# Performance work log

Hardware: AMD Instinct MI355X
Metric: run time of the kernel (lower is better)

Reference implementation:

```python
import jax, jax.numpy as jnp
import numpy as np
from jax import lax

STRIDES = [8, 16, 32, 64, 128]
NUM_CLASSES = 80
PRE_NMS_THRESH = 0.05
PRE_NMS_TOP_N = 1000
NMS_THRESH = 0.6
MAX_DET = 100
IMG_SIZE = 800.0
BBOX_W = (10.0, 10.0, 5.0, 5.0)
SCALE_CLAMP = float(np.log(1000.0 / 16.0))  # Box2BoxTransform clamp


def conv3x3(x, w, b):
    y = lax.conv_general_dilated(x, w, (1, 1), 'SAME',
                                 dimension_numbers=('NCHW', 'OIHW', 'NCHW'))
    return y + b[None, :, None, None]


def conv1x1(x, w, b):
    return jnp.einsum('nchw,kc->nkhw', x, w) + b[None, :, None, None]


def make_anchors(H, W, stride):
    # one square anchor per location, size = 8 * stride (ATSS), offset 0.5
    size = 8.0 * stride
    xs = (jnp.arange(W, dtype=jnp.float32) + 0.5) * stride
    ys = (jnp.arange(H, dtype=jnp.float32) + 0.5) * stride
    cy, cx = jnp.meshgrid(ys, xs, indexing='ij')
    half = size / 2.0
    return jnp.stack([cx - half, cy - half, cx + half, cy + half], -1).reshape(-1, 4)


def decode(deltas, anchors):
    # Box2BoxTransform.apply_deltas with weights (10,10,5,5)
    wx, wy, ww, wh = BBOX_W
    aw = anchors[..., 2] - anchors[..., 0]
    ah = anchors[..., 3] - anchors[..., 1]
    acx = anchors[..., 0] + 0.5 * aw
    acy = anchors[..., 1] + 0.5 * ah
    dx = deltas[..., 0] / wx
    dy = deltas[..., 1] / wy
    dw = jnp.minimum(deltas[..., 2] / ww, SCALE_CLAMP)
    dh = jnp.minimum(deltas[..., 3] / wh, SCALE_CLAMP)
    pcx = dx * aw + acx
    pcy = dy * ah + acy
    pw = jnp.exp(dw) * aw
    ph = jnp.exp(dh) * ah
    boxes = jnp.stack([pcx - 0.5 * pw, pcy - 0.5 * ph,
                       pcx + 0.5 * pw, pcy + 0.5 * ph], -1)
    return jnp.clip(boxes, 0.0, IMG_SIZE)


def iou_one_vs_all(box, boxes):
    x1 = jnp.maximum(box[0], boxes[:, 0])
    y1 = jnp.maximum(box[1], boxes[:, 1])
    x2 = jnp.minimum(box[2], boxes[:, 2])
    y2 = jnp.minimum(box[3], boxes[:, 3])
    inter = jnp.clip(x2 - x1, 0.0) * jnp.clip(y2 - y1, 0.0)
    a1 = (box[2] - box[0]) * (box[3] - box[1])
    a2 = (boxes[:, 2] - boxes[:, 0]) * (boxes[:, 3] - boxes[:, 1])
    return inter / (a1 + a2 - inter + 1e-9)


def nms_single(boxes, scores, classes):
    # class-aware greedy NMS via per-class coordinate offset (ml_nms trick)
    off = classes.astype(boxes.dtype)[:, None] * (2.0 * IMG_SIZE)
    ob = boxes + off

    def step(s, _):
        i = jnp.argmax(s)
        best = s[i]
        iou = iou_one_vs_all(ob[i], ob)
        s = jnp.where(iou > NMS_THRESH, -1.0, s)
        s = s.at[i].set(-1.0)
        return s, (i, best)

    _, (idx, kept) = lax.scan(step, scores, None, length=MAX_DET)
    valid = kept > 0
    out_boxes = jnp.where(valid[:, None], boxes[idx], 0.0)
    out_scores = jnp.where(valid, kept, 0.0)
    out_classes = jnp.where(valid, classes[idx], -1)
    return out_boxes, out_scores, out_classes


def atss_forward(feats, cls_tw, cls_tb, bbox_tw, bbox_tb,
                 wcls, bcls, wbox, bbox_b, wctr, bctr, scales):
    all_boxes, all_scores, all_classes = [], [], []
    for l, x in enumerate(feats):
        c = x
        b = x
        for i in range(cls_tw.shape[0]):  # 4 tower convs
            c = jax.nn.relu(conv3x3(c, cls_tw[i], cls_tb[i]))
            b = jax.nn.relu(conv3x3(b, bbox_tw[i], bbox_tb[i]))
        logits = conv1x1(c, wcls, bcls)               # [N,C,H,W]
        deltas = scales[l] * conv1x1(b, wbox, bbox_b)  # [N,4,H,W]
        ctr = conv1x1(b, wctr, bctr)                   # [N,1,H,W]
        N, C, H, W = logits.shape
        logits = logits.transpose(0, 2, 3, 1).reshape(N, H * W, C)
        deltas = deltas.transpose(0, 2, 3, 1).reshape(N, H * W, 4)
        ctr = ctr.transpose(0, 2, 3, 1).reshape(N, H * W)
        anchors = make_anchors(H, W, STRIDES[l])       # [HW,4]
        # ATSS inference scoring: sigmoid(cls) * sigmoid(centerness)
        s = jax.nn.sigmoid(logits) * jax.nn.sigmoid(ctr)[..., None]
        s = jnp.where(s > PRE_NMS_THRESH, s, 0.0)
        flat = s.reshape(N, -1)                        # [N, HW*C]
        k = min(PRE_NMS_TOP_N, flat.shape[1])
        vals, idx = lax.top_k(flat, k)
        aidx = idx // C
        cidx = idx % C
        d = jnp.take_along_axis(deltas, aidx[:, :, None], axis=1)  # [N,k,4]
        boxes = decode(d, anchors[aidx])
        # final score = sqrt(cls*ctr); safe sqrt to avoid inf grad at 0
        sc = jnp.sqrt(jnp.where(vals > 0, vals, 1.0)) * (vals > 0)
        all_boxes.append(boxes)
        all_scores.append(sc)
        all_classes.append(cidx)
    boxes = jnp.concatenate(all_boxes, 1)
    scores = jnp.concatenate(all_scores, 1)
    classes = jnp.concatenate(all_classes, 1)
    return jax.vmap(nms_single)(boxes, scores, classes)


def setup_inputs() -> dict:
    key = jax.random.key(0)
    ks = jax.random.split(key, 12)
    feats_hw = [(100, 100), (50, 50), (25, 25), (13, 13), (7, 7)]
    N, CIN, CH = 4, 256, 256
    inp = {}
    for i, (h, w) in enumerate(feats_hw):
        inp['p%d' % (i + 3)] = jax.random.normal(ks[i], (N, CIN, h, w), jnp.float32)
    inp['cls_tw'] = jax.random.normal(ks[5], (4, CH, CIN, 3, 3), jnp.float32) * 0.02
    inp['cls_tb'] = jnp.zeros((4, CH), jnp.float32)
    inp['bbox_tw'] = jax.random.normal(ks[6], (4, CH, CIN, 3, 3), jnp.float32) * 0.02
    inp['bbox_tb'] = jnp.zeros((4, CH), jnp.float32)
    inp['wcls'] = jax.random.normal(ks[7], (NUM_CLASSES, CH), jnp.float32) * 0.05
    inp['bcls'] = jnp.zeros((NUM_CLASSES,), jnp.float32)
    inp['wbox'] = jax.random.normal(ks[8], (4, CH), jnp.float32) * 0.05
    inp['bbox_b'] = jnp.zeros((4,), jnp.float32)
    inp['wctr'] = jax.random.normal(ks[9], (1, CH), jnp.float32) * 0.05
    inp['bctr'] = jnp.zeros((1,), jnp.float32)
    inp['scales'] = jnp.ones((5,), jnp.float32)
    return inp


def reference(p3, p4, p5, p6, p7, cls_tw, cls_tb, bbox_tw, bbox_tb,
              wcls, bcls, wbox, bbox_b, wctr, bctr, scales):
    feats = [p3, p4, p5, p6, p7]
    boxes, scores, classes = atss_forward(feats, cls_tw, cls_tb, bbox_tw, bbox_tb,
                                          wcls, bcls, wbox, bbox_b, wctr, bctr, scales)
    return boxes, scores, classes
```

## Files before the change

kernel.cpp:

```cpp
#include <hip/hip_runtime.h>
#include <math.h>

typedef short s8v __attribute__((ext_vector_type(8)));
typedef short s4v __attribute__((ext_vector_type(4)));
typedef float f4v __attribute__((ext_vector_type(4)));
typedef _Float16 h8v __attribute__((ext_vector_type(8)));

__device__ __forceinline__ float sigf(float x) { return 1.f / (1.f + expf(-x)); }
__device__ __forceinline__ float f16f(short v) {
  return (float)__builtin_bit_cast(_Float16, v);
}

#define SCALE_CLAMP 4.135166556742356f
#define IMG_SIZE 800.f
#define PLANE 14482432ull
#define W_SCALE 1024.f
#define A_SCALE 64.f
#define ACC_RESCALE 1.52587890625e-5f

__device__ __forceinline__ void split2(float x, short& h, short& l) {
  _Float16 hf = (_Float16)x;
  _Float16 lf = (_Float16)(x - (float)hf);
  h = __builtin_bit_cast(short, hf);
  l = __builtin_bit_cast(short, lf);
}

struct Geo {
  int tp[6];
  int TXa[5];
  int Ha[5], Wa[5], PWa[5], PHWa[5];
  int phwOff[5];
  int hwOff[5];
  int pb[6];
  int bb[6];
};

__global__ __launch_bounds__(256) void wtrans_k(const float* __restrict__ cls_tw,
                                                const float* __restrict__ bbox_tw,
                                                short* __restrict__ wt)
{
  const int total = 589824;
  for (int u = blockIdx.x * 256 + threadIdx.x; u < total; u += gridDim.x * 256) {
    int layer = u / 73728;
    int r = u - layer * 73728;
    int tap = r / 8192;  r -= tap * 8192;
    int cc  = r / 1024;  r -= cc * 1024;
    int qq  = r / 256;   int ko = r - qq * 256;
    int cibase = cc * 32 + qq * 8;
    const float* src = (layer < 4) ? (cls_tw + (size_t)layer * 589824)
                                   : (bbox_tw + (size_t)(layer - 4) * 589824);
    s8v hv, lv;
#pragma unroll
    for (int e = 0; e < 8; ++e) {
      float x = src[(size_t)ko * 2304 + (size_t)(cibase + e) * 9 + tap] * W_SCALE;
      short h, l; split2(x, h, l);
      hv[e] = h; lv[e] = l;
    }
    size_t dbase = (size_t)layer * 1179648 + (((size_t)tap * 8 + cc) * 4 + qq) * 2048 + (size_t)ko * 8;
    *(s8v*)(wt + dbase) = hv;
    *(s8v*)(wt + dbase + 589824) = lv;
  }
}

__global__ __launch_bounds__(256) void prep_all_k(const float* __restrict__ p3, const float* __restrict__ p4,
                                                  const float* __restrict__ p5, const float* __restrict__ p6,
                                                  const float* __restrict__ p7,
                                                  short* __restrict__ out, Geo g)
{
  __shared__ float tl[64][260];
  int bx = blockIdx.x, t = threadIdx.x, n = blockIdx.y;
  int l = 0; while (l < 4 && bx >= g.pb[l + 1]) ++l;
  const float* in = (l == 0) ? p3 : (l == 1) ? p4 : (l == 2) ? p5 : (l == 3) ? p6 : p7;
  int H = g.Ha[l], W = g.Wa[l], PW = g.PWa[l], PHW = g.PHWa[l], HW = H * W;
  int P0 = (bx - g.pb[l]) * 64;
  const float* inN = in + (size_t)n * HW * 256;
  int sub = t >> 6, pl = t & 63;
  int pos = P0 + pl;
  for (int i = 0; i < 64; ++i) {
    int ci = i * 4 + sub;
    tl[pl][ci] = (pos < HW) ? inN[(size_t)ci * HW + pos] : 0.f;
  }
  __syncthreads();
  int pl2 = t >> 2, cq = (t & 3) * 64;
  int pos2 = P0 + pl2;
  if (pos2 < HW) {
    int y = pos2 / W, x = pos2 - y * W;
    size_t oo = ((size_t)g.phwOff[l] * 4 + (size_t)n * PHW + (size_t)(y + 1) * PW + (x + 1)) * 256 + cq;
#pragma unroll
    for (int grp = 0; grp < 8; ++grp) {
      s8v hv, lv;
#pragma unroll
      for (int e = 0; e < 8; ++e) {
        short h, lo; split2(tl[pl2][cq + grp * 8 + e] * A_SCALE, h, lo);
        hv[e] = h; lv[e] = lo;
      }
      *(s8v*)(out + oo + grp * 8) = hv;
      *(s8v*)(out + PLANE + oo + grp * 8) = lv;
    }
  }
}

#define QS    128
#define PSTR  4096
#define BSTR  8192
__global__ __launch_bounds__(256, 4) void conv_all_k(const short* __restrict__ in0,
                                                     const short* __restrict__ wtL,
                                                     const float* __restrict__ bias,
                                                     short* __restrict__ out0, Geo g)
{
  __shared__ short act_s[2 * BSTR];

  const int t = threadIdx.x;
  const int lane = t & 63, wave = t >> 6;
  const int wcol = wave & 1, wko = wave >> 1;
  const int nT = g.tp[5];
  int bid = blockIdx.x;
  int wgid = (bid & 7) * nT + (bid >> 3);
  const int n = wgid / (2 * nT);
  int r2 = wgid - n * 2 * nT;
  int bx = r2 >> 1;
  const int ko0 = (r2 & 1) * 128;
  int l = 0; while (l < 4 && bx >= g.tp[l + 1]) ++l;
  const int H = g.Ha[l], W = g.Wa[l], PW = g.PWa[l], PHW = g.PHWa[l];
  const int lt = bx - g.tp[l];
  const int TX = g.TXa[l];
  const int ty = lt / TX, tx = lt - ty * TX;
  const int R0 = ty * 4, C0 = tx * 16;
  const size_t bi = ((size_t)g.phwOff[l] * 4 + (size_t)n * PHW) * 256;
  const short* inN = in0 + bi;
  short* outN = out0 + bi;

  const int r = lane & 15, q = lane >> 4;
  const int cb = wcol * 8;
  const short* wlane = wtL + (size_t)q * 2048 + (size_t)(ko0 + wko * 64 + r) * 8;
  const int abase = q * QS + 2 * q + (r >> 3) * 18 + cb + (r & 7);

  int soff[2];
#pragma unroll
  for (int k = 0; k < 2; ++k) {
    int j = t + k * 256;
    int qq = j >> 7, ppos = j & 127;
    int lpos = ppos - 2 * qq;
    if (lpos < 0) lpos = 0;
    if (lpos > 107) lpos = 107;
    int row = lpos / 18, col = lpos - row * 18;
    int prow = R0 + row; if (prow > H + 1) prow = H + 1;
    int pcol = C0 + col; if (pcol > W + 1) pcol = W + 1;
    soff[k] = (prow * PW + pcol) * 256 + qq * 8;
  }

  f4v acc[2][4];
#pragma unroll
  for (int mi = 0; mi < 2; ++mi)
#pragma unroll
    for (int ni = 0; ni < 4; ++ni) { f4v z = {0.f, 0.f, 0.f, 0.f}; acc[mi][ni] = z; }

  auto stage = [&](int cc, int buf) {
#pragma unroll
    for (int k = 0; k < 2; ++k)
#pragma unroll
      for (int p = 0; p < 2; ++p) {
        const short* src = inN + (size_t)p * PLANE + (size_t)(soff[k] + cc * 32);
        short* dst = &act_s[(size_t)buf * BSTR + (size_t)p * PSTR + (size_t)(t + k * 256) * 8];
#if __has_builtin(__builtin_amdgcn_global_load_lds)
        __builtin_amdgcn_global_load_lds((const __attribute__((address_space(1))) void*)src,
                                         (__attribute__((address_space(3))) void*)dst, 16, 0, 0);
#else
        *(s8v*)dst = *(const s8v*)src;
#endif
      }
  };

  auto loadW = [&](s8v (&w)[2][2], int cc2, int tap2, int half) {
    const short* base = wlane + (size_t)(tap2 * 8 + cc2) * 8192 + half * 256;
#pragma unroll
    for (int p = 0; p < 2; ++p)
#pragma unroll
      for (int k = 0; k < 2; ++k)
        w[p][k] = *(const s8v*)(base + (size_t)p * 589824 + k * 128);
  };

  auto loadA = [&](s8v (&af)[2][2], int dy, int dx, int buf) {
    const int b0 = buf * BSTR + abase * 8;
    const int d = (dy * 18 + dx) * 8;
#pragma unroll
    for (int mi = 0; mi < 2; ++mi) {
      af[0][mi] = *(const s8v*)&act_s[b0 + mi * 288 + d];
      af[1][mi] = *(const s8v*)&act_s[b0 + PSTR + mi * 288 + d];
    }
  };

  auto runHalf = [&](const s8v (&w)[2][2], const s8v (&af)[2][2], int half) {
    const int PA[3] = {0, 0, 1};
    const int PB[3] = {0, 1, 0};
    __builtin_amdgcn_s_setprio(1);
#pragma unroll
    for (int pp = 0; pp < 3; ++pp)
#pragma unroll
      for (int mi = 0; mi < 2; ++mi)
#pragma unroll
        for (int k = 0; k < 2; ++k)
          acc[mi][half * 2 + k] = __builtin_amdgcn_mfma_f32_16x16x32_f16(
              __builtin_bit_cast(h8v, af[PA[pp]][mi]),
              __builtin_bit_cast(h8v, w[PB[pp]][k]),
              acc[mi][half * 2 + k], 0, 0, 0);
    __builtin_amdgcn_s_setprio(0);
  };

  s8v wH0[2][2], wH1[2][2], afr[2][2];
  stage(0, 0);
  loadW(wH0, 0, 0, 0);
  __syncthreads();

  int cur = 0;
  for (int cc = 0; cc < 8; ++cc) {
    if (cc < 7) stage(cc + 1, cur ^ 1);
#pragma unroll
    for (int tap = 0; tap < 9; ++tap) {
      const int dy = tap / 3, dx = tap - dy * 3;
      loadW(wH1, cc, tap, 1);
      loadA(afr, dy, dx, cur);
      runHalf(wH0, afr, 0);
      int ntap = tap + 1, ncc = cc;
      if (ntap == 9) { ntap = 0; ++ncc; }
      if (ncc < 8) loadW(wH0, ncc, ntap, 0);
      runHalf(wH1, afr, 1);
    }
    __syncthreads();
    cur ^= 1;
  }

#pragma unroll
  for (int mi = 0; mi < 2; ++mi) {
#pragma unroll
    for (int ni = 0; ni < 4; ++ni) {
      int ko = ko0 + wko * 64 + ni * 16 + r;
      float bv = bias[ko];
#pragma unroll
      for (int reg = 0; reg < 4; ++reg) {
        int rm = q * 4 + reg;
        int orow = R0 + 2 * mi + (rm >> 3);
        int ocol = C0 + cb + (rm & 7);
        if (orow < H && ocol < W) {
          float real = acc[mi][ni][reg] * ACC_RESCALE + bv;
          float vv = fmaxf(real, 0.f) * A_SCALE;
          short h, lo; split2(vv, h, lo);
          size_t oo = ((size_t)(orow + 1) * PW + (ocol + 1)) * 256 + ko;
          outN[oo] = h; outN[PLANE + oo] = lo;
        }
      }
    }
  }
}

__global__ __launch_bounds__(256) void cls_head_k(const short* __restrict__ act,
                                                  const float* __restrict__ wcls,
                                                  const float* __restrict__ bcls,
                                                  float* __restrict__ score, Geo g)
{
  __shared__ int   p2s[64];
  __shared__ float as_[64][69];
  __shared__ float ws_[64][84];
  const int t = threadIdx.x;
  const int n = blockIdx.y;
  int bx = blockIdx.x;
  int l = 0; while (l < 4 && bx >= g.pb[l + 1]) ++l;
  const int H = g.Ha[l], W = g.Wa[l], PW = g.PWa[l], PHW = g.PHWa[l], HW = H * W;
  const int P0 = (bx - g.pb[l]) * 64;
  if (t < 64) {
    int p = P0 + t; if (p >= HW) p = HW - 1;
    int y = p / W, x = p - y * W;
    p2s[t] = (y + 1) * PW + x + 1;
  }
  __syncthreads();
  float accv[4][5];
#pragma unroll
  for (int i = 0; i < 4; ++i)
#pragma unroll
    for (int j = 0; j < 5; ++j) accv[i][j] = 0.f;

  const short* actN = act + ((size_t)g.phwOff[l] * 4 + (size_t)n * PHW) * 256;
  const int pg = t >> 4, cg = t & 15;
  const float inv = 1.f / A_SCALE;

  for (int c0 = 0; c0 < 256; c0 += 64) {
    for (int i = t; i < 1024; i += 256) {
      int pos = i >> 4, c4 = i & 15;
      size_t o = (size_t)p2s[pos] * 256 + c0 + c4 * 4;
      s4v hv = *(const s4v*)(actN + o);
      s4v lv = *(const s4v*)(actN + PLANE + o);
      float* dst = &as_[pos][c4 * 4];
#pragma unroll
      for (int e = 0; e < 4; ++e) dst[e] = (f16f(hv[e]) + f16f(lv[e])) * inv;
    }
    for (int i = t; i < 1280; i += 256) {
      int c = i >> 4, c4 = i & 15;
      float4 v = *(const float4*)(wcls + (size_t)c * 256 + c0 + c4 * 4);
      ws_[c4 * 4 + 0][c] = v.x; ws_[c4 * 4 + 1][c] = v.y;
      ws_[c4 * 4 + 2][c] = v.z; ws_[c4 * 4 + 3][c] = v.w;
    }
    __syncthreads();
#pragma unroll 8
    for (int ci = 0; ci < 64; ++ci) {
#pragma unroll
      for (int i = 0; i < 4; ++i) {
        float a = as_[pg * 4 + i][ci];
#pragma unroll
        for (int j = 0; j < 5; ++j)
          accv[i][j] = fmaf(a, ws_[ci][cg * 5 + j], accv[i][j]);
      }
    }
    __syncthreads();
  }
  float* sB = score + ((size_t)g.hwOff[l] * 4 + (size_t)n * HW) * 80;
#pragma unroll
  for (int i = 0; i < 4; ++i) {
    int p = P0 + pg * 4 + i;
    if (p >= HW) continue;
#pragma unroll
    for (int j = 0; j < 5; ++j) {
      int c = cg * 5 + j;
      sB[(size_t)p * 80 + c] = sigf(accv[i][j] + bcls[c]);
    }
  }
}

__global__ __launch_bounds__(256) void box_head_k(const short* __restrict__ act,
                                                  const float* __restrict__ wbox,
                                                  const float* __restrict__ bb,
                                                  const float* __restrict__ wctr,
                                                  const float* __restrict__ bc,
                                                  const float* __restrict__ scales,
                                                  float* __restrict__ score,
                                                  float* __restrict__ deltas, Geo g)
{
  int n = blockIdx.y;
  int bx = blockIdx.x;
  int l = 0; while (l < 4 && bx >= g.bb[l + 1]) ++l;
  const int H = g.Ha[l], W = g.Wa[l], PW = g.PWa[l], PHW = g.PHWa[l], HW = H * W;
  int p = (bx - g.bb[l]) * 256 + threadIdx.x;
  if (p >= HW) return;
  int y = p / W, x = p - y * W;
  const short* a = act + ((size_t)g.phwOff[l] * 4 + (size_t)n * PHW + (size_t)(y + 1) * PW + x + 1) * 256;
  const float inv = 1.f / A_SCALE;
  float d0 = 0, d1 = 0, d2 = 0, d3 = 0, ct = 0;
  for (int gI = 0; gI < 32; ++gI) {
    s8v hv = *(const s8v*)(a + gI * 8);
    s8v lv = *(const s8v*)(a + PLANE + gI * 8);
#pragma unroll
    for (int e = 0; e < 8; ++e) {
      float av = (f16f(hv[e]) + f16f(lv[e])) * inv;
      int c = gI * 8 + e;
      d0 = fmaf(av, wbox[c], d0);
      d1 = fmaf(av, wbox[256 + c], d1);
      d2 = fmaf(av, wbox[512 + c], d2);
      d3 = fmaf(av, wbox[768 + c], d3);
      ct = fmaf(av, wctr[c], ct);
    }
  }
  float sl = scales[l];
  float* dd = deltas + ((size_t)g.hwOff[l] * 4 + (size_t)n * HW + p) * 4;
  dd[0] = sl * (d0 + bb[0]); dd[1] = sl * (d1 + bb[1]);
  dd[2] = sl * (d2 + bb[2]); dd[3] = sl * (d3 + bb[3]);
  float sct = sigf(ct + bc[0]);
  float* sp = score + ((size_t)g.hwOff[l] * 4 + (size_t)n * HW + p) * 80;
#pragma unroll
  for (int i = 0; i < 20; ++i) {
    float4 v = ((float4*)sp)[i];
    v.x *= sct; v.y *= sct; v.z *= sct; v.w *= sct;
    v.x = (v.x > 0.05f) ? v.x : 0.f;
    v.y = (v.y > 0.05f) ? v.y : 0.f;
    v.z = (v.z > 0.05f) ? v.z : 0.f;
    v.w = (v.w > 0.05f) ? v.w : 0.f;
    ((float4*)sp)[i] = v;
  }
}

__global__ __launch_bounds__(256) void hist_k(const float* __restrict__ score,
                                              const unsigned* __restrict__ thr,
                                              unsigned* __restrict__ hist, int phase, Geo g)
{
  const int grp = blockIdx.y;
  const int l = grp >> 2, n = grp & 3;
  const int HW = g.Ha[l] * g.Wa[l];
  const int M = HW * 80;
  const float* s = score + ((size_t)g.hwOff[l] * 4 + (size_t)n * HW) * 80;
  unsigned* h = hist + grp * 2048;
  const unsigned* tr = thr + grp * 8;
  __shared__ unsigned lh[2048];
  for (int i = threadIdx.x; i < 2048; i += 256) lh[i] = 0u;
  __syncthreads();
  unsigned B1 = 0, pref = 0;
  if (phase == 1) B1 = tr[0];
  if (phase == 2) pref = (tr[0] << 11) | tr[1];
  for (int idx = blockIdx.x * 256 + threadIdx.x; idx < M; idx += gridDim.x * 256) {
    float v = s[idx];
    if (v > 0.f) {
      unsigned b = __float_as_uint(v);
      if (phase == 0) atomicAdd(&lh[b >> 20], 1u);
      else if (phase == 1) { if ((b >> 20) == B1) atomicAdd(&lh[(b >> 9) & 0x7FFu], 1u); }
      else { if ((b >> 9) == pref) atomicAdd(&lh[b & 0x1FFu], 1u); }
    }
  }
  __syncthreads();
  for (int i = threadIdx.x; i < 2048; i += 256) { unsigned v = lh[i]; if (v) atomicAdd(&h[i], v); }
}

__global__ __launch_bounds__(256) void scan_k(unsigned* __restrict__ hist,
                                              unsigned* __restrict__ thr, int phase)
{
  const int grp = blockIdx.x, t = threadIdx.x;
  unsigned* h  = hist + grp * 2048;
  unsigned* tr = thr + grp * 8;
  const int nb = (phase == 2) ? 512 : 2048;
  const int PB = nb / 256;
  unsigned target = 1000u;
  bool dead = false;
  if (phase >= 1) {
    target = 1000u - tr[2];
    if (tr[0] == 0xFFFFFFFFu) dead = true;
    if (phase == 2 && tr[1] == 0xFFFFFFFFu) dead = true;
  }
  __shared__ unsigned ps[256];
  __shared__ unsigned s_tot;
  const int hi = nb - t * PB;
  unsigned lsum = 0;
  for (int k = 0; k < PB; ++k) lsum += h[hi - 1 - k];
  ps[t] = lsum;
  __syncthreads();
  if (t == 0) {
    unsigned cum = 0;
    for (int i = 0; i < 256; ++i) { unsigned tmp = ps[i]; ps[i] = cum; cum += tmp; }
    s_tot = cum;
  }
  __syncthreads();
  unsigned exc = ps[t], tot = s_tot;
  if (!dead && tot >= target) {
    if (exc < target && exc + lsum >= target) {
      unsigned cum = exc; int bf = 0; unsigned above = 0;
      for (int k = 0; k < PB; ++k) {
        int bidx = hi - 1 - k;
        unsigned c = h[bidx];
        if (cum < target && cum + c >= target) { bf = bidx; above = cum; }
        cum += c;
      }
      if (phase == 0)      { tr[0] = (unsigned)bf; tr[2] = above; }
      else if (phase == 1) { tr[1] = (unsigned)bf; tr[2] = tr[2] + above; }
      else {
        unsigned T = (tr[0] << 20) | (tr[1] << 9) | (unsigned)bf;
        tr[3] = T; tr[4] = target - above;
      }
    }
  } else if (t == 0) {
    if (phase == 0)      { tr[0] = 0xFFFFFFFFu; tr[2] = 0u; }
    else if (phase == 1) { tr[1] = 0xFFFFFFFFu; }
    else                 { tr[3] = 0u; tr[4] = 0u; }
  }
  if (phase == 2 && t == 0) { tr[5] = 0u; tr[6] = 0u; }
}

__global__ __launch_bounds__(256) void select_k(const float* __restrict__ score,
                                                const float* __restrict__ deltas,
                                                unsigned* __restrict__ thr,
                                                float* __restrict__ cbox, float* __restrict__ csc,
                                                float* __restrict__ ccls, float* __restrict__ cgid,
                                                Geo g)
{
  const int grp = blockIdx.y;
  const int l = grp >> 2, n = grp & 3;
  const int W = g.Wa[l];
  const int HW = g.Ha[l] * W;
  const int M = HW * 80;
  const float stride_ = (float)(8 << l);
  const float* s = score + ((size_t)g.hwOff[l] * 4 + (size_t)n * HW) * 80;
  const float* dBase = deltas + ((size_t)g.hwOff[l] * 4 + (size_t)n * HW) * 4;
  unsigned* tr = thr + grp * 8;
  const unsigned T = tr[3], need = tr[4];
  for (int idx = blockIdx.x * 256 + threadIdx.x; idx < M; idx += gridDim.x * 256) {
    float v = s[idx];
    if (!(v > 0.f)) continue;
    unsigned b = __float_as_uint(v);
    int slot = -1;
    if (b > T) slot = (int)atomicAdd(&tr[5], 1u);
    else if (b == T) {
      unsigned e = atomicAdd(&tr[6], 1u);
      if (e < need) slot = (int)(1000u - need + e);
    }
    if (slot < 0) continue;
    int p = idx / 80, c = idx - p * 80;
    int y = p / W, x = p - y * W;
    const float* d = dBase + (size_t)p * 4;
    float sz  = 8.f * stride_;
    float acx = ((float)x + 0.5f) * stride_;
    float acy = ((float)y + 0.5f) * stride_;
    float dx = d[0] / 10.f, dy = d[1] / 10.f;
    float dw = fminf(d[2] / 5.f, SCALE_CLAMP);
    float dh = fminf(d[3] / 5.f, SCALE_CLAMP);
    float pcx = dx * sz + acx;
    float pcy = dy * sz + acy;
    float pw = expf(dw) * sz;
    float ph = expf(dh) * sz;
    float x1 = pcx - 0.5f * pw, y1_ = pcy - 0.5f * ph;
    float x2 = pcx + 0.5f * pw, y2_ = pcy + 0.5f * ph;
    x1  = fminf(fmaxf(x1, 0.f),  IMG_SIZE);
    y1_ = fminf(fmaxf(y1_, 0.f), IMG_SIZE);
    x2  = fminf(fmaxf(x2, 0.f),  IMG_SIZE);
    y2_ = fminf(fmaxf(y2_, 0.f), IMG_SIZE);
    int cslot = n * 5000 + l * 1000 + slot;
    ((float4*)cbox)[cslot] = make_float4(x1, y1_, x2, y2_);
    csc[cslot]  = sqrtf(v);
    ccls[cslot] = (float)c;
    cgid[cslot] = (float)(((unsigned)l << 20) | (unsigned)idx);
  }
}

__global__ __launch_bounds__(256) void nms_bucket_k(const float* __restrict__ cbox,
                                                    const float* __restrict__ csc,
                                                    const float* __restrict__ ccls,
                                                    const float* __restrict__ cgid,
                                                    float4* __restrict__ bbox2,
                                                    unsigned long long* __restrict__ bkey2,
                                                    int* __restrict__ coff)
{
  __shared__ unsigned cnt[80];
  __shared__ unsigned off_s[81];
  const int n = blockIdx.x, t = threadIdx.x;
  for (int i = t; i < 80; i += 256) cnt[i] = 0u;
  __syncthreads();
  for (int i = t; i < 5000; i += 256) {
    float s = csc[n * 5000 + i];
    if (s > 0.f) atomicAdd(&cnt[(int)ccls[n * 5000 + i]], 1u);
  }
  __syncthreads();
  if (t == 0) {
    unsigned c = 0;
    for (int k = 0; k < 80; ++k) { off_s[k] = c; c += cnt[k]; }
    off_s[80] = c;
  }
  __syncthreads();
  for (int i = t; i < 81; i += 256) coff[n * 81 + i] = (int)off_s[i];
  for (int i = t; i < 80; i += 256) cnt[i] = 0u;
  __syncthreads();
  for (int i = t; i < 5000; i += 256) {
    float s = csc[n * 5000 + i];
    if (s > 0.f) {
      int c = (int)ccls[n * 5000 + i];
      unsigned p = atomicAdd(&cnt[c], 1u);
      int dst = n * 5000 + (int)off_s[c] + (int)p;
      bbox2[dst] = ((const float4*)cbox)[n * 5000 + i];
      unsigned long long sb = (unsigned long long)__float_as_uint(s);
      unsigned gid = (unsigned)cgid[n * 5000 + i];
      bkey2[dst] = (sb << 24) | (unsigned long long)(0xFFFFFFu - gid);
    }
  }
}

#define NCAP 1536
__global__ __launch_bounds__(64) void nms_class_k(const float4* __restrict__ bbox2,
                                                  unsigned long long* __restrict__ bkey2,
                                                  const int* __restrict__ coff,
                                                  float4* __restrict__ kbox,
                                                  unsigned long long* __restrict__ kkey,
                                                  int* __restrict__ kcnt)
{
  __shared__ unsigned long long key_s[NCAP];
  __shared__ unsigned long long sk_s[NCAP];
  __shared__ float4 sb_s[NCAP];
  __shared__ unsigned char af_s[NCAP + 64];
  const int cls = blockIdx.x, n = blockIdx.y, t = threadIdx.x;
  const int lo = coff[n * 81 + cls], hi = coff[n * 81 + cls + 1];
  const int c = hi - lo;
  const int base = n * 5000 + lo;
  const int outB = (n * 80 + cls) * 100;
  int kept = 0;
  if (c > 0 && c <= NCAP) {
    const int nch = (c + 63) >> 6;
    for (int i = t; i < nch * 64; i += 64) af_s[i] = 0;
    for (int i = t; i < c; i += 64) key_s[i] = bkey2[base + i];
    __syncthreads();
    for (int i = t; i < c; i += 64) {
      unsigned long long ki = key_s[i];
      int rk = 0;
      for (int m = 0; m < c; ++m) rk += (key_s[m] > ki) ? 1 : 0;
      sk_s[rk] = ki;
      sb_s[rk] = bbox2[base + i];
      af_s[rk] = 1;
    }
    __syncthreads();
    int p = -1;
    while (kept < 100) {
      int np = -1;
      int j0 = (p + 1) >> 6;
      for (int j = j0; j < nch; ++j) {
        int pos = j * 64 + t;
        unsigned long long w = __ballot(af_s[pos] != 0);
        if (j == j0) { int sh = (p + 1) & 63; if (sh) w &= (~0ull) << sh; }
        if (w) { np = j * 64 + (int)__builtin_ctzll(w); break; }
      }
      if (np < 0) break;
      p = np;
      float4 wb = sb_s[p];
      if (t == 0) { kbox[outB + kept] = wb; kkey[outB + kept] = sk_s[p]; }
      ++kept;
      float a1 = (wb.z - wb.x) * (wb.w - wb.y);
      for (int i = p + t; i < c; i += 64) {
        if (!af_s[i]) continue;
        float4 b = sb_s[i];
        float xx1 = fmaxf(wb.x, b.x), yy1 = fmaxf(wb.y, b.y);
        float xx2 = fminf(wb.z, b.z), yy2 = fminf(wb.w, b.w);
        float inter = fmaxf(xx2 - xx1, 0.f) * fmaxf(yy2 - yy1, 0.f);
        float a2 = (b.z - b.x) * (b.w - b.y);
        if (inter / (a1 + a2 - inter + 1e-9f) > 0.6f) af_s[i] = 0;
      }
      __syncthreads();
    }
  } else if (c > NCAP) {
    while (kept < 100) {
      unsigned long long best = 0ull; int bi = 0;
      for (int i = t; i < c; i += 64) {
        unsigned long long k = bkey2[base + i];
        if (k > best) { best = k; bi = i; }
      }
#pragma unroll
      for (int o = 32; o; o >>= 1) {
        unsigned long long ok = __shfl_xor(best, o);
        int oi = __shfl_xor(bi, o);
        if (ok > best) { best = ok; bi = oi; }
      }
      if (best == 0ull) break;
      float4 wb = bbox2[base + bi];
      if (t == 0) { kbox[outB + kept] = wb; kkey[outB + kept] = best; }
      ++kept;
      float a1 = (wb.z - wb.x) * (wb.w - wb.y);
      for (int i = t; i < c; i += 64) {
        unsigned long long k = bkey2[base + i];
        if (!k) continue;
        float4 b = bbox2[base + i];
        float xx1 = fmaxf(wb.x, b.x), yy1 = fmaxf(wb.y, b.y);
        float xx2 = fminf(wb.z, b.z), yy2 = fminf(wb.w, b.w);
        float inter = fmaxf(xx2 - xx1, 0.f) * fmaxf(yy2 - yy1, 0.f);
        float a2 = (b.z - b.x) * (b.w - b.y);
        if (inter / (a1 + a2 - inter + 1e-9f) > 0.6f) bkey2[base + i] = 0ull;
      }
      __syncthreads();
    }
  }
  if (t == 0) kcnt[n * 80 + cls] = kept;
}

__global__ __launch_bounds__(64) void nms_merge_k(const float4* __restrict__ kbox,
                                                  const unsigned long long* __restrict__ kkey,
                                                  const int* __restrict__ kcnt,
                                                  float* __restrict__ outp)
{
  __shared__ unsigned long long lk[8000];
  __shared__ int head[80];
  __shared__ int cnts[80];
  const int n = blockIdx.x, t = threadIdx.x;
  for (int i = t; i < 80; i += 64) { head[i] = 0; cnts[i] = kcnt[n * 80 + i]; }
  for (int i = t; i < 8000; i += 64) lk[i] = kkey[n * 8000 + i];
  __syncthreads();
  for (int it = 0; it < 100; ++it) {
    unsigned long long best = 0ull; int bc = 0;
    for (int cls = t; cls < 80; cls += 64) {
      int h = head[cls];
      if (h < cnts[cls]) {
        unsigned long long k = lk[cls * 100 + h];
        if (k > best) { best = k; bc = cls; }
      }
    }
#pragma unroll
    for (int o = 32; o; o >>= 1) {
      unsigned long long ok = __shfl_xor(best, o);
      int oc = __shfl_xor(bc, o);
      if (ok > best) { best = ok; bc = oc; }
    }
    if (t == 0) {
      int basei = n * 100 + it;
      if (best != 0ull) {
        int idx = (n * 80 + bc) * 100 + head[bc];
        float4 b = kbox[idx];
        outp[basei * 4 + 0] = b.x; outp[basei * 4 + 1] = b.y;
        outp[basei * 4 + 2] = b.z; outp[basei * 4 + 3] = b.w;
        outp[1600 + basei] = __uint_as_float((unsigned)(best >> 24));
        outp[2000 + basei] = (float)bc;
        head[bc] = head[bc] + 1;
      } else {
        outp[basei * 4 + 0] = 0.f; outp[basei * 4 + 1] = 0.f;
        outp[basei * 4 + 2] = 0.f; outp[basei * 4 + 3] = 0.f;
        outp[1600 + basei] = 0.f;
        outp[2000 + basei] = -1.f;
      }
    }
    __syncthreads();
  }
}

extern "C" void kernel_launch(void* const* d_in, const int* in_sizes, int n_in,
                              void* d_out, int out_size, void* d_ws, size_t ws_size,
                              hipStream_t stream)
{
  (void)in_sizes; (void)n_in; (void)out_size; (void)ws_size;
  const float* p3 = (const float*)d_in[0];
  const float* p4 = (const float*)d_in[1];
  const float* p5 = (const float*)d_in[2];
  const float* p6 = (const float*)d_in[3];
  const float* p7 = (const float*)d_in[4];
  const float* cls_tw  = (const float*)d_in[5];
  const float* cls_tb  = (const float*)d_in[6];
  const float* bbox_tw = (const float*)d_in[7];
  const float* bbox_tb = (const float*)d_in[8];
  const float* wcls    = (const float*)d_in[9];
  const float* bcls    = (const float*)d_in[10];
  const float* wbox    = (const float*)d_in[11];
  const float* bbox_b  = (const float*)d_in[12];
  const float* wctr    = (const float*)d_in[13];
  const float* bctr    = (const float*)d_in[14];
  const float* scales  = (const float*)d_in[15];
  float* out = (float*)d_out;

  Geo G;
  const int Hs[5] = {100, 50, 25, 13, 7};
  {
    int tpre = 0, ppre = 0, bpre = 0, phw = 0, hw = 0;
    for (int l = 0; l < 5; ++l) {
      int H = Hs[l], W = Hs[l];
      G.Ha[l] = H; G.Wa[l] = W; G.PWa[l] = W + 2; G.PHWa[l] = (H + 2) * (W + 2);
      G.TXa[l] = (W + 15) / 16;
      int TY = (H + 3) / 4;
      G.tp[l] = tpre;  tpre += G.TXa[l] * TY;
      G.pb[l] = ppre;  ppre += (H * W + 63) / 64;
      G.bb[l] = bpre;  bpre += (H * W + 255) / 256;
      G.phwOff[l] = phw; phw += G.PHWa[l];
      G.hwOff[l]  = hw;  hw  += H * W;
    }
    G.tp[5] = tpre; G.pb[5] = ppre; G.bb[5] = bpre;
  }
  const int nTiles = G.tp[5];
  const int nPrep  = G.pb[5];
  const int nBoxB  = G.bb[5];
  const int sumHW = 13343;
  const size_t scoreBytes  = (size_t)sumHW * 4 * 80 * 4;
  const size_t deltasBytes = (size_t)sumHW * 4 * 4 * 4;

  char* ws = (char*)d_ws;
  size_t off = 0;
  auto alloc = [&](size_t bytes) -> void* {
    off = (off + 255) & ~(size_t)255;
    void* p = ws + off; off += bytes; return p;
  };
  const size_t bufBytes = 2ull * PLANE * 2;

  short* wt     = (short*)alloc((size_t)8 * 2 * 589824 * 2);
  float* cbox   = (float*)alloc(4ull * 5000 * 4 * 4);
  float* csc    = (float*)alloc(4ull * 5000 * 4);
  float* ccls   = (float*)alloc(4ull * 5000 * 4);
  float* cgid   = (float*)alloc(4ull * 5000 * 4);
  unsigned* hist = (unsigned*)alloc(20ull * 2048 * 4);
  unsigned* thr  = (unsigned*)alloc(20ull * 8 * 4);
  float4* bbox2 = (float4*)alloc(4ull * 5000 * 16);
  unsigned long long* bkey2 = (unsigned long long*)alloc(4ull * 5000 * 8);
  int* coff     = (int*)alloc(4ull * 81 * 4);
  float4* kbox  = (float4*)alloc(320ull * 100 * 16);
  unsigned long long* kkey = (unsigned long long*)alloc(320ull * 100 * 8);
  int* kcnt     = (int*)alloc(320ull * 4);
  short* C = (short*)alloc(bufBytes);
  short* A = (short*)alloc(bufBytes);
  short* B = (short*)alloc(bufBytes);
  float* score  = (float*)alloc(scoreBytes);
  float* deltas = (float*)alloc(deltasBytes);

  hipMemsetAsync(csc,  0, 4ull * 5000 * 4, stream);
  hipMemsetAsync(ccls, 0, 4ull * 5000 * 4, stream);
  hipMemsetAsync(cgid, 0, 4ull * 5000 * 4, stream);
  hipMemsetAsync(thr,  0, 20ull * 8 * 4, stream);
  hipMemsetAsync(C, 0, bufBytes, stream);
  hipMemsetAsync(A, 0, bufBytes, stream);
  hipMemsetAsync(B, 0, bufBytes, stream);

  wtrans_k<<<1024, 256, 0, stream>>>(cls_tw, bbox_tw, wt);

  const size_t LSTRIDE = 2ull * 589824;
  dim3 cg(8 * nTiles);

  prep_all_k<<<dim3(nPrep, 4), 256, 0, stream>>>(p3, p4, p5, p6, p7, C, G);
  conv_all_k<<<cg, 256, 0, stream>>>(C, wt + 0 * LSTRIDE, cls_tb + 0 * 256, A, G);
  conv_all_k<<<cg, 256, 0, stream>>>(A, wt + 1 * LSTRIDE, cls_tb + 1 * 256, B, G);
  conv_all_k<<<cg, 256, 0, stream>>>(B, wt + 2 * LSTRIDE, cls_tb + 2 * 256, A, G);
  conv_all_k<<<cg, 256, 0, stream>>>(A, wt + 3 * LSTRIDE, cls_tb + 3 * 256, B, G);
  cls_head_k<<<dim3(nPrep, 4), 256, 0, stream>>>(B, wcls, bcls, score, G);
  conv_all_k<<<cg, 256, 0, stream>>>(C, wt + 4 * LSTRIDE, bbox_tb + 0 * 256, A, G);
  conv_all_k<<<cg, 256, 0, stream>>>(A, wt + 5 * LSTRIDE, bbox_tb + 1 * 256, C, G);
  conv_all_k<<<cg, 256, 0, stream>>>(C, wt + 6 * LSTRIDE, bbox_tb + 2 * 256, A, G);
  conv_all_k<<<cg, 256, 0, stream>>>(A, wt + 7 * LSTRIDE, bbox_tb + 3 * 256, C, G);
  box_head_k<<<dim3(nBoxB, 4), 256, 0, stream>>>(C, wbox, bbox_b, wctr, bctr, scales,
                                                 score, deltas, G);

  const int hb = 196;
  for (int phase = 0; phase < 3; ++phase) {
    hipMemsetAsync(hist, 0, 20ull * 2048 * 4, stream);
    hist_k<<<dim3(hb, 20), 256, 0, stream>>>(score, thr, hist, phase, G);
    scan_k<<<20, 256, 0, stream>>>(hist, thr, phase);
  }
  select_k<<<dim3(hb, 20), 256, 0, stream>>>(score, deltas, thr, cbox, csc, ccls, cgid, G);

  nms_bucket_k<<<4, 256, 0, stream>>>(cbox, csc, ccls, cgid, bbox2, bkey2, coff);
  nms_class_k<<<dim3(80, 4), 64, 0, stream>>>(bbox2, bkey2, coff, kbox, kkey, kcnt);
  nms_merge_k<<<4, 64, 0, stream>>>(kbox, kkey, kcnt, out);
}
```

Measured before the change: 2.165 ms.

## Prefetch full next-tap weights into ping-pong registers in conv kernel

Restructures the conv main loop so each tap loads the full set of weight fragments for the next tap into an alternating register buffer, instead of splitting weights into two halves. Each tap now runs all of its MFMAs back to back, with a scheduling barrier keeping the prefetch loads ahead of the compute. The channel-chunk loop is unrolled in pairs so the buffer roles swap statically. This needs more registers, so the launch bound drops from 4 to 3 waves per SIMD, trading occupancy for deeper load latency hiding.

```diff
diff --git a/kernel.cpp b/kernel.cpp
--- a/kernel.cpp
+++ b/kernel.cpp
@@ -103,7 +103,7 @@
 #define QS    128
 #define PSTR  4096
 #define BSTR  8192
-__global__ __launch_bounds__(256, 4) void conv_all_k(const short* __restrict__ in0,
+__global__ __launch_bounds__(256, 3) void conv_all_k(const short* __restrict__ in0,
                                                      const short* __restrict__ wtL,
                                                      const float* __restrict__ bias,
                                                      short* __restrict__ out0, Geo g)
@@ -171,26 +171,24 @@
       }
   };
 
-  auto loadW = [&](s8v (&w)[2][2], int cc2, int tap2, int half) {
-    const short* base = wlane + (size_t)(tap2 * 8 + cc2) * 8192 + half * 256;
+  auto loadWT = [&](s8v (&w)[2][4], int cc2, int tap2) {
+    const short* base = wlane + (size_t)(tap2 * 8 + cc2) * 8192;
 #pragma unroll
     for (int p = 0; p < 2; ++p)
 #pragma unroll
-      for (int k = 0; k < 2; ++k)
+      for (int k = 0; k < 4; ++k)
         w[p][k] = *(const s8v*)(base + (size_t)p * 589824 + k * 128);
   };
 
-  auto loadA = [&](s8v (&af)[2][2], int dy, int dx, int buf) {
+  auto runTap = [&](const s8v (&w)[2][4], int dy, int dx, int buf) {
+    s8v afr[2][2];
     const int b0 = buf * BSTR + abase * 8;
     const int d = (dy * 18 + dx) * 8;
 #pragma unroll
     for (int mi = 0; mi < 2; ++mi) {
-      af[0][mi] = *(const s8v*)&act_s[b0 + mi * 288 + d];
-      af[1][mi] = *(const s8v*)&act_s[b0 + PSTR + mi * 288 + d];
-    }
-  };
-
-  auto runHalf = [&](const s8v (&w)[2][2], const s8v (&af)[2][2], int half) {
+      afr[0][mi] = *(const s8v*)&act_s[b0 + mi * 288 + d];
+      afr[1][mi] = *(const s8v*)&act_s[b0 + PSTR + mi * 288 + d];
+    }
     const int PA[3] = {0, 0, 1};
     const int PB[3] = {0, 1, 0};
     __builtin_amdgcn_s_setprio(1);
@@ -199,34 +197,46 @@
 #pragma unroll
       for (int mi = 0; mi < 2; ++mi)
 #pragma unroll
-        for (int k = 0; k < 2; ++k)
-          acc[mi][half * 2 + k] = __builtin_amdgcn_mfma_f32_16x16x32_f16(
-              __builtin_bit_cast(h8v, af[PA[pp]][mi]),
-              __builtin_bit_cast(h8v, w[PB[pp]][k]),
-              acc[mi][half * 2 + k], 0, 0, 0);
+        for (int ni = 0; ni < 4; ++ni)
+          acc[mi][ni] = __builtin_amdgcn_mfma_f32_16x16x32_f16(
+              __builtin_bit_cast(h8v, afr[PA[pp]][mi]),
+              __builtin_bit_cast(h8v, w[PB[pp]][ni]),
+              acc[mi][ni], 0, 0, 0);
     __builtin_amdgcn_s_setprio(0);
   };
 
-  s8v wH0[2][2], wH1[2][2], afr[2][2];
-  stage(0, 0);
-  loadW(wH0, 0, 0, 0);
-  __syncthreads();
-
-  int cur = 0;
-  for (int cc = 0; cc < 8; ++cc) {
-    if (cc < 7) stage(cc + 1, cur ^ 1);
+  s8v wA[2][4], wB[2][4];
+
+  auto ccBody = [&](int cc, int buf, s8v (&wF)[2][4], s8v (&wS)[2][4]) {
+    if (cc < 7) stage(cc + 1, buf ^ 1);
 #pragma unroll
     for (int tap = 0; tap < 9; ++tap) {
       const int dy = tap / 3, dx = tap - dy * 3;
-      loadW(wH1, cc, tap, 1);
-      loadA(afr, dy, dx, cur);
-      runHalf(wH0, afr, 0);
-      int ntap = tap + 1, ncc = cc;
-      if (ntap == 9) { ntap = 0; ++ncc; }
-      if (ncc < 8) loadW(wH0, ncc, ntap, 0);
-      runHalf(wH1, afr, 1);
+      int ntap = (tap == 8) ? 0 : tap + 1;
+      int ncc  = (tap == 8) ? cc + 1 : cc;
+      if ((tap & 1) == 0) {
+        if (ncc < 8) loadWT(wS, ncc, ntap);
+        __builtin_amdgcn_sched_barrier(0);
+        runTap(wF, dy, dx, buf);
+      } else {
+        if (ncc < 8) loadWT(wF, ncc, ntap);
+        __builtin_amdgcn_sched_barrier(0);
+        runTap(wS, dy, dx, buf);
+      }
     }
     __syncthreads();
+  };
+
+  stage(0, 0);
+  loadWT(wA, 0, 0);
+  __syncthreads();
+
+  int cur = 0;
+#pragma unroll
+  for (int ccp = 0; ccp < 4; ++ccp) {
+    ccBody(2 * ccp, cur, wA, wB);
+    cur ^= 1;
+    ccBody(2 * ccp + 1, cur, wB, wA);
     cur ^= 1;
   }
 
```

After: 2.177 ms. About the same (+0.6%).
